# Kernel tuning notes

Measured on AMD Instinct MI355X. Metric: run time of the kernel, lower is better.

Reference implementation:

```python
import jax, jax.numpy as jnp
import numpy as np

H = 4            # num_heads (forced: 128 projection / d_k=32)
DK = 32          # hardcoded d_k
SCALE = 1.0 / np.sqrt(32.0)
EPS = 1e-5       # LayerNorm eps (torch default)


def setup_inputs() -> dict:
    key = jax.random.key(0)
    ks = jax.random.split(key, 8)
    B, L, Dq, Dkv, M = 16, 4096, 512, 512, 512
    def w(k, shape, fan_in):
        return (jax.random.normal(k, shape, jnp.float32) / np.sqrt(fan_in)).astype(jnp.float32)
    return {
        "Q_in":  jax.random.normal(ks[0], (B, L, Dq),  jnp.float32),
        "KV_in": jax.random.normal(ks[1], (B, L, Dkv), jnp.float32),
        "Wq":  w(ks[2], (Dq, 128), Dq),   "bq":  jnp.zeros((128,), jnp.float32),
        "Wk":  w(ks[3], (Dkv, 128), Dkv), "bk":  jnp.zeros((128,), jnp.float32),
        "Wv":  w(ks[4], (Dkv, 128), Dkv), "bv":  jnp.zeros((128,), jnp.float32),
        "Wo":  w(ks[5], (128, M), 128),   "bo":  jnp.zeros((M,), jnp.float32),
        "Wqo": w(ks[6], (128, M), 128),   "bqo": jnp.zeros((M,), jnp.float32),
        "gamma": jnp.ones((M,), jnp.float32),
        "beta":  jnp.zeros((M,), jnp.float32),
    }


def reference(Q_in, KV_in, Wq, bq, Wk, bk, Wv, bv, Wo, bo, Wqo, bqo, gamma, beta):
    B, L, _ = Q_in.shape
    Qm = Q_in @ Wq + bq          # (B, L, 128)
    Km = KV_in @ Wk + bk         # (B, L, 128)
    Vm = KV_in @ Wv + bv         # (B, L, 128)

    def heads(X):
        # view(B, L, H, DK).permute(0, 2, 3, 1) -> (B, H, DK, L)
        return X.reshape(B, L, H, DK).transpose(0, 2, 3, 1)

    Qh, Kh, Vh = heads(Qm), heads(Km), heads(Vm)
    # matmul contracts over the SEQUENCE dim -> feature-feature scores (B,H,DK,DK)
    scores = jnp.einsum('bhdl,bhel->bhde', Qh, Kh) * SCALE
    attn = jax.nn.softmax(scores, axis=-1)          # dropout = identity (eval)
    out_h = jnp.einsum('bhde,bhel->bhdl', attn, Vh)  # (B, H, DK, L)
    out_h = out_h.transpose(0, 3, 1, 2).reshape(B, L, H * DK)  # (B, L, 128)

    out = out_h @ Wo + bo        # (B, L, M)
    Qm_ = Qm @ Wqo + bqo         # (B, L, M)
    x = Qm_ + out
    mu = jnp.mean(x, axis=-1, keepdims=True)
    var = jnp.var(x, axis=-1, keepdims=True)
    y = (x - mu) * jax.lax.rsqrt(var + EPS) * gamma + beta
    return (y, attn)
```

## Files before the change

kernel.cpp:

```cpp
#include <hip/hip_runtime.h>
#include <hip/hip_bf16.h>

typedef __bf16   bf16x8 __attribute__((ext_vector_type(8)));
typedef _Float16 f16x8  __attribute__((ext_vector_type(8)));
typedef float    f32x4  __attribute__((ext_vector_type(4)));

#define SCALE_QK 0.17677669529663687f
#define LDSS 40
#define TL   136

__device__ __forceinline__ float b2f(ushort u) {
    __hip_bfloat16 h; *reinterpret_cast<ushort*>(&h) = u; return __bfloat162float(h);
}
__device__ __forceinline__ ushort f2b(float f) {
    __hip_bfloat16 h = __float2bfloat16(f); return *reinterpret_cast<ushort*>(&h);
}
__device__ __forceinline__ ushort f2h(float f) {
    union { _Float16 h; ushort u; } x; x.h = (_Float16)f; return x.u;
}

__global__ void k_prep(const float* __restrict__ Wq, const float* __restrict__ Wk,
                       const float* __restrict__ Wv, const float* __restrict__ Wqo,
                       const float* __restrict__ Wo,
                       ushort* __restrict__ WqT, ushort* __restrict__ WkT,
                       ushort* __restrict__ WvT, ushort* __restrict__ WqoT,
                       ushort* __restrict__ WoB) {
    int idx = blockIdx.x * 256 + threadIdx.x;
    int mat = idx >> 16, i = idx & 65535;
    if (mat == 0) {
        int n = i >> 9, k = i & 511;
        WqT[i] = f2h(Wq[k * 128 + n]);
    } else if (mat == 1) {
        int n = i >> 9, k = i & 511;
        WkT[i] = f2h(Wk[k * 128 + n]);
    } else if (mat == 2) {
        int n = i >> 9, k = i & 511;
        WvT[i] = f2h(Wv[k * 128 + n]);
    } else if (mat == 3) {
        int n = i >> 7, k = i & 127;
        WqoT[i] = f2b(Wqo[k * 512 + n]);
    } else if (mat == 4) {
        WoB[i] = f2b(Wo[i]);
    }
}

__global__ __launch_bounds__(256) void k_qkv_scores(
        const float* __restrict__ Qin, const float* __restrict__ KVin,
        const ushort* __restrict__ WqT, const ushort* __restrict__ WkT,
        const ushort* __restrict__ WvT,
        const float* __restrict__ bq, const float* __restrict__ bk,
        const float* __restrict__ bv,
        ushort* __restrict__ QmB, ushort* __restrict__ VmB,
        float* __restrict__ partial) {
    __shared__ __align__(16) ushort lds[2 * 128 * TL];
    ushort* P1  = lds;
    ushort* P2  = lds + 128 * TL;
    ushort* As  = P2;
    ushort* Bs0 = P2 + 128 * LDSS;
    ushort* Bs1 = P2 + 2 * 128 * LDSS;

    const int row0 = blockIdx.x * 128;
    const int tid  = threadIdx.x;
    const int wid  = tid >> 6, lane = tid & 63;
    const int wm = wid >> 1, wn = wid & 1;
    const int quad = lane >> 4, l16 = lane & 15;
    const int sr = tid >> 2;
    const int sc = (tid & 3) * 8;

    {
        f32x4 acc[4][4] = {};
        for (int k0 = 0; k0 < 512; k0 += 32) {
            __syncthreads();
#pragma unroll
            for (int p = 0; p < 2; ++p) {
                int r = sr + p * 64;
                float4 a0 = *(const float4*)&Qin[(size_t)(row0 + r) * 512 + k0 + sc];
                float4 a1 = *(const float4*)&Qin[(size_t)(row0 + r) * 512 + k0 + sc + 4];
                union { uint4 v; ushort u[8]; } H;
                H.u[0] = f2h(a0.x); H.u[1] = f2h(a0.y); H.u[2] = f2h(a0.z); H.u[3] = f2h(a0.w);
                H.u[4] = f2h(a1.x); H.u[5] = f2h(a1.y); H.u[6] = f2h(a1.z); H.u[7] = f2h(a1.w);
                *(uint4*)&As[r * LDSS + sc]  = H.v;
                *(uint4*)&Bs0[r * LDSS + sc] = *(const uint4*)&WqT[(size_t)r * 512 + k0 + sc];
            }
            __syncthreads();
            f16x8 aF[4];
#pragma unroll
            for (int i = 0; i < 4; ++i)
                aF[i] = *reinterpret_cast<const f16x8*>(&As[(wm * 64 + i * 16 + l16) * LDSS + quad * 8]);
#pragma unroll
            for (int j = 0; j < 4; ++j) {
                f16x8 bF = *reinterpret_cast<const f16x8*>(&Bs0[(wn * 64 + j * 16 + l16) * LDSS + quad * 8]);
#pragma unroll
                for (int i = 0; i < 4; ++i)
                    acc[i][j] = __builtin_amdgcn_mfma_f32_16x16x32_f16(aF[i], bF, acc[i][j], 0, 0, 0);
            }
        }
#pragma unroll
        for (int j = 0; j < 4; ++j) {
            int col = wn * 64 + j * 16 + l16;
            float bqv = bq[col];
#pragma unroll
            for (int i = 0; i < 4; ++i)
#pragma unroll
                for (int r = 0; r < 4; ++r) {
                    int row = wm * 64 + i * 16 + quad * 4 + r;
                    float v = acc[i][j][r] + bqv;
                    QmB[(size_t)(row0 + row) * 128 + col] = f2b(v);
                    P1[col * TL + row] = f2h(v);
                }
        }
    }

    {
        f32x4 accK[4][4] = {};
        f32x4 accV[4][4] = {};
        for (int k0 = 0; k0 < 512; k0 += 32) {
            __syncthreads();
#pragma unroll
            for (int p = 0; p < 2; ++p) {
                int r = sr + p * 64;
                float4 a0 = *(const float4*)&KVin[(size_t)(row0 + r) * 512 + k0 + sc];
                float4 a1 = *(const float4*)&KVin[(size_t)(row0 + r) * 512 + k0 + sc + 4];
                union { uint4 v; ushort u[8]; } H;
                H.u[0] = f2h(a0.x); H.u[1] = f2h(a0.y); H.u[2] = f2h(a0.z); H.u[3] = f2h(a0.w);
                H.u[4] = f2h(a1.x); H.u[5] = f2h(a1.y); H.u[6] = f2h(a1.z); H.u[7] = f2h(a1.w);
                *(uint4*)&As[r * LDSS + sc]  = H.v;
                *(uint4*)&Bs0[r * LDSS + sc] = *(const uint4*)&WkT[(size_t)r * 512 + k0 + sc];
                *(uint4*)&Bs1[r * LDSS + sc] = *(const uint4*)&WvT[(size_t)r * 512 + k0 + sc];
            }
            __syncthreads();
            f16x8 aF[4];
#pragma unroll
            for (int i = 0; i < 4; ++i)
                aF[i] = *reinterpret_cast<const f16x8*>(&As[(wm * 64 + i * 16 + l16) * LDSS + quad * 8]);
#pragma unroll
            for (int j = 0; j < 4; ++j) {
                f16x8 bK = *reinterpret_cast<const f16x8*>(&Bs0[(wn * 64 + j * 16 + l16) * LDSS + quad * 8]);
                f16x8 bV = *reinterpret_cast<const f16x8*>(&Bs1[(wn * 64 + j * 16 + l16) * LDSS + quad * 8]);
#pragma unroll
                for (int i = 0; i < 4; ++i) {
                    accK[i][j] = __builtin_amdgcn_mfma_f32_16x16x32_f16(aF[i], bK, accK[i][j], 0, 0, 0);
                    accV[i][j] = __builtin_amdgcn_mfma_f32_16x16x32_f16(aF[i], bV, accV[i][j], 0, 0, 0);
                }
            }
        }
        __syncthreads();
#pragma unroll
        for (int j = 0; j < 4; ++j) {
            int col = wn * 64 + j * 16 + l16;
            float bkv = bk[col], bvv = bv[col];
#pragma unroll
            for (int i = 0; i < 4; ++i)
#pragma unroll
                for (int r = 0; r < 4; ++r) {
                    int row = wm * 64 + i * 16 + quad * 4 + r;
                    float vv = accV[i][j][r] + bvv;
                    VmB[(size_t)(row0 + row) * 128 + col] = f2b(vv);
                    P2[col * TL + row] = f2h(accK[i][j][r] + bkv);
                }
        }
    }
    __syncthreads();

    {
        const int h = wid;
        f32x4 s[2][2] = {};
#pragma unroll
        for (int ks = 0; ks < 4; ++ks) {
            f16x8 qa[2], kb[2];
#pragma unroll
            for (int dt = 0; dt < 2; ++dt)
                qa[dt] = *reinterpret_cast<const f16x8*>(
                    &P1[(h * 32 + dt * 16 + l16) * TL + ks * 32 + quad * 8]);
#pragma unroll
            for (int et = 0; et < 2; ++et)
                kb[et] = *reinterpret_cast<const f16x8*>(
                    &P2[(h * 32 + et * 16 + l16) * TL + ks * 32 + quad * 8]);
#pragma unroll
            for (int dt = 0; dt < 2; ++dt)
#pragma unroll
                for (int et = 0; et < 2; ++et)
                    s[dt][et] = __builtin_amdgcn_mfma_f32_16x16x32_f16(qa[dt], kb[et], s[dt][et], 0, 0, 0);
        }
        const int b = blockIdx.x >> 5, sp = blockIdx.x & 31;
        float* P = partial + (size_t)(sp * 64 + b * 4 + h) * 1024;
#pragma unroll
        for (int dt = 0; dt < 2; ++dt)
#pragma unroll
            for (int et = 0; et < 2; ++et)
#pragma unroll
                for (int r = 0; r < 4; ++r) {
                    int d = dt * 16 + quad * 4 + r, e = et * 16 + l16;
                    P[d * 32 + e] = s[dt][et][r];
                }
    }
}

__global__ __launch_bounds__(256) void k_attn(
        const float* __restrict__ partial, const ushort* __restrict__ WoB,
        float* __restrict__ attnOut, ushort* __restrict__ WcT) {
    int bh = blockIdx.x; int b = bh >> 2, h = bh & 3;
    __shared__ float aS[1024];
    __shared__ __align__(16) ushort wS[32 * 512];
    int t = threadIdx.x;
    for (int i = t; i < 1024; i += 256) {
        float s = 0.f;
#pragma unroll
        for (int sp = 0; sp < 32; ++sp)
            s += partial[(size_t)(sp * 64 + bh) * 1024 + i];
        aS[i] = s * SCALE_QK;
    }
    for (int i = t; i < 2048; i += 256) {
        int r = i >> 6, c = (i & 63) * 8;
        *(uint4*)&wS[r * 512 + c] = *(const uint4*)&WoB[(size_t)(h * 32 + r) * 512 + c];
    }
    __syncthreads();
    if (t < 32) {
        float m = -1e30f;
#pragma unroll
        for (int e = 0; e < 32; ++e) m = fmaxf(m, aS[t * 32 + e]);
        float p[32]; float sum = 0.f;
#pragma unroll
        for (int e = 0; e < 32; ++e) { p[e] = __expf(aS[t * 32 + e] - m); sum += p[e]; }
        float inv = 1.f / sum;
#pragma unroll
        for (int e = 0; e < 32; ++e) aS[t * 32 + e] = p[e] * inv;
    }
    __syncthreads();
    for (int i = t; i < 1024; i += 256)
        attnOut[(size_t)bh * 1024 + i] = aS[i];
    int e = t & 31, mg = t >> 5;
    for (int mi = 0; mi < 64; ++mi) {
        int m = mg * 64 + mi;
        float acc = 0.f;
#pragma unroll
        for (int d = 0; d < 32; ++d)
            acc += aS[d * 32 + e] * b2f(wS[d * 512 + m]);
        WcT[((size_t)b * 512 + m) * 128 + h * 32 + e] = f2b(acc);
    }
}

__global__ __launch_bounds__(256) void k_out_ln(
        const ushort* __restrict__ Vm, const ushort* __restrict__ Qm,
        const ushort* __restrict__ WcT, const ushort* __restrict__ WqoT,
        const float* __restrict__ bo, const float* __restrict__ bqo,
        const float* __restrict__ gamma, const float* __restrict__ beta,
        float* __restrict__ Y) {
    __shared__ __align__(16) ushort As[64 * LDSS];
    __shared__ __align__(16) ushort Bs[512 * LDSS];
    __shared__ float sumS[4][64], sumSS[4][64], muA[64], rsA[64];
    const int row0 = blockIdx.x * 64;
    const int b = row0 >> 12;
    const ushort* WcTb = WcT + (size_t)b * 512 * 128;
    const int tid = threadIdx.x;
    const int wid = tid >> 6, lane = tid & 63;
    const int quad = lane >> 4, l16 = lane & 15;
    const int sr = tid >> 2;
    const int sc = (tid & 3) * 8;

    f32x4 acc[4][8] = {};

    for (int k0 = 0; k0 < 256; k0 += 32) {
        const ushort* Asrc; const ushort* Bsrc; int kk;
        if (k0 < 128) { Asrc = Vm; Bsrc = WcTb; kk = k0; }
        else          { Asrc = Qm; Bsrc = WqoT; kk = k0 - 128; }
        __syncthreads();
        *(uint4*)&As[sr * LDSS + sc] =
            *(const uint4*)&Asrc[(size_t)(row0 + sr) * 128 + kk + sc];
#pragma unroll
        for (int p = 0; p < 8; ++p) {
            int r = sr + p * 64;
            *(uint4*)&Bs[r * LDSS + sc] = *(const uint4*)&Bsrc[(size_t)r * 128 + kk + sc];
        }
        __syncthreads();
        bf16x8 aF[4];
#pragma unroll
        for (int i = 0; i < 4; ++i)
            aF[i] = *reinterpret_cast<const bf16x8*>(&As[(i * 16 + l16) * LDSS + quad * 8]);
#pragma unroll
        for (int j = 0; j < 8; ++j) {
            bf16x8 bF = *reinterpret_cast<const bf16x8*>(
                &Bs[(wid * 128 + j * 16 + l16) * LDSS + quad * 8]);
#pragma unroll
            for (int i = 0; i < 4; ++i)
                acc[i][j] = __builtin_amdgcn_mfma_f32_16x16x32_bf16(aF[i], bF, acc[i][j], 0, 0, 0);
        }
    }

    float bv[8];
#pragma unroll
    for (int j = 0; j < 8; ++j) {
        int ncol = wid * 128 + j * 16 + l16;
        bv[j] = bo[ncol] + bqo[ncol];
    }
    float sArr[4][4], ssArr[4][4];
#pragma unroll
    for (int i = 0; i < 4; ++i)
#pragma unroll
        for (int r = 0; r < 4; ++r) {
            float s = 0.f, ss = 0.f;
#pragma unroll
            for (int j = 0; j < 8; ++j) {
                float x = acc[i][j][r] + bv[j];
                s += x; ss += x * x;
            }
            sArr[i][r] = s; ssArr[i][r] = ss;
        }
#pragma unroll
    for (int off = 1; off < 16; off <<= 1)
#pragma unroll
        for (int i = 0; i < 4; ++i)
#pragma unroll
            for (int r = 0; r < 4; ++r) {
                sArr[i][r]  += __shfl_xor(sArr[i][r],  off, 64);
                ssArr[i][r] += __shfl_xor(ssArr[i][r], off, 64);
            }
    if (l16 == 0) {
#pragma unroll
        for (int i = 0; i < 4; ++i)
#pragma unroll
            for (int r = 0; r < 4; ++r) {
                int row = i * 16 + quad * 4 + r;
                sumS[wid][row]  = sArr[i][r];
                sumSS[wid][row] = ssArr[i][r];
            }
    }
    __syncthreads();
    if (tid < 64) {
        float s = sumS[0][tid] + sumS[1][tid] + sumS[2][tid] + sumS[3][tid];
        float ss = sumSS[0][tid] + sumSS[1][tid] + sumSS[2][tid] + sumSS[3][tid];
        float mu = s * (1.f / 512.f);
        float var = ss * (1.f / 512.f) - mu * mu;
        muA[tid] = mu;
        rsA[tid] = rsqrtf(var + 1e-5f);
    }
    __syncthreads();

    float gj[8], bj[8];
#pragma unroll
    for (int j = 0; j < 8; ++j) {
        int ncol = wid * 128 + j * 16 + l16;
        gj[j] = gamma[ncol]; bj[j] = beta[ncol];
    }
#pragma unroll
    for (int i = 0; i < 4; ++i)
#pragma unroll
        for (int r = 0; r < 4; ++r) {
            int row = i * 16 + quad * 4 + r;
            float mu = muA[row], rstd = rsA[row];
            size_t base = (size_t)(row0 + row) * 512 + wid * 128 + l16;
#pragma unroll
            for (int j = 0; j < 8; ++j) {
                float x = acc[i][j][r] + bv[j];
                Y[base + j * 16] = (x - mu) * rstd * gj[j] + bj[j];
            }
        }
}

extern "C" void kernel_launch(void* const* d_in, const int* in_sizes, int n_in,
                              void* d_out, int out_size, void* d_ws, size_t ws_size,
                              hipStream_t stream) {
    const float* Qin   = (const float*)d_in[0];
    const float* KVin  = (const float*)d_in[1];
    const float* Wq    = (const float*)d_in[2];
    const float* bq    = (const float*)d_in[3];
    const float* Wk    = (const float*)d_in[4];
    const float* bk    = (const float*)d_in[5];
    const float* Wv    = (const float*)d_in[6];
    const float* bv    = (const float*)d_in[7];
    const float* Wo    = (const float*)d_in[8];
    const float* bo    = (const float*)d_in[9];
    const float* Wqo   = (const float*)d_in[10];
    const float* bqo   = (const float*)d_in[11];
    const float* gamma = (const float*)d_in[12];
    const float* beta  = (const float*)d_in[13];
    float* out = (float*)d_out;
    float* attnOut = out + 33554432;

    char* ws = (char*)d_ws;
    ushort* WqT  = (ushort*)(ws);
    ushort* WkT  = (ushort*)(ws + 131072);
    ushort* WvT  = (ushort*)(ws + 262144);
    ushort* WqoT = (ushort*)(ws + 393216);
    ushort* WoB  = (ushort*)(ws + 524288);
    ushort* QmB  = (ushort*)(ws + 655360);
    ushort* VmB  = (ushort*)(ws + 17432576);
    float*  part = (float*) (ws + 34209792);
    ushort* WcT  = (ushort*)(ws + 42598400);

    k_prep<<<1280, 256, 0, stream>>>(Wq, Wk, Wv, Wqo, Wo,
                                     WqT, WkT, WvT, WqoT, WoB);
    k_qkv_scores<<<512, 256, 0, stream>>>(Qin, KVin, WqT, WkT, WvT,
                                          bq, bk, bv, QmB, VmB, part);
    k_attn<<<64, 256, 0, stream>>>(part, WoB, attnOut, WcT);
    k_out_ln<<<1024, 256, 0, stream>>>(VmB, QmB, WcT, WqoT, bo, bqo, gamma, beta, out);
}
```

Baseline: 434.5 us.

## Load GEMM fragments directly from global memory and parallelize attn softmax kernel

Removes LDS staging and the per-k-step barriers in the QKV projection and output/LayerNorm GEMMs, so each wave loads its MFMA fragments straight from global memory (with f32-to-f16 conversion in registers). This drops the sync and LDS traffic cost but gives up LDS data sharing, so waves in the same block reload the same A/B rows, leaning on L1/L2. The attn kernel is split across 4 blocks along the output dimension, its softmax is spread over all threads with shuffles, and it caches the attention column in registers and the Wo slice in LDS as float.

```diff
diff --git a/kernel.cpp b/kernel.cpp
--- a/kernel.cpp
+++ b/kernel.cpp
@@ -6,7 +6,6 @@
 typedef float    f32x4  __attribute__((ext_vector_type(4)));
 
 #define SCALE_QK 0.17677669529663687f
-#define LDSS 40
 #define TL   136
 
 __device__ __forceinline__ float b2f(ushort u) {
@@ -17,6 +16,12 @@
 }
 __device__ __forceinline__ ushort f2h(float f) {
     union { _Float16 h; ushort u; } x; x.h = (_Float16)f; return x.u;
+}
+__device__ __forceinline__ f16x8 cvt8f(float4 a, float4 b) {
+    union { f16x8 v; ushort u[8]; } H;
+    H.u[0] = f2h(a.x); H.u[1] = f2h(a.y); H.u[2] = f2h(a.z); H.u[3] = f2h(a.w);
+    H.u[4] = f2h(b.x); H.u[5] = f2h(b.y); H.u[6] = f2h(b.z); H.u[7] = f2h(b.w);
+    return H.v;
 }
 
 __global__ void k_prep(const float* __restrict__ Wq, const float* __restrict__ Wk,
@@ -53,43 +58,29 @@
         ushort* __restrict__ QmB, ushort* __restrict__ VmB,
         float* __restrict__ partial) {
     __shared__ __align__(16) ushort lds[2 * 128 * TL];
-    ushort* P1  = lds;
-    ushort* P2  = lds + 128 * TL;
-    ushort* As  = P2;
-    ushort* Bs0 = P2 + 128 * LDSS;
-    ushort* Bs1 = P2 + 2 * 128 * LDSS;
+    ushort* P1 = lds;
+    ushort* P2 = lds + 128 * TL;
 
     const int row0 = blockIdx.x * 128;
     const int tid  = threadIdx.x;
     const int wid  = tid >> 6, lane = tid & 63;
     const int wm = wid >> 1, wn = wid & 1;
     const int quad = lane >> 4, l16 = lane & 15;
-    const int sr = tid >> 2;
-    const int sc = (tid & 3) * 8;
 
     {
         f32x4 acc[4][4] = {};
+#pragma unroll 4
         for (int k0 = 0; k0 < 512; k0 += 32) {
-            __syncthreads();
-#pragma unroll
-            for (int p = 0; p < 2; ++p) {
-                int r = sr + p * 64;
-                float4 a0 = *(const float4*)&Qin[(size_t)(row0 + r) * 512 + k0 + sc];
-                float4 a1 = *(const float4*)&Qin[(size_t)(row0 + r) * 512 + k0 + sc + 4];
-                union { uint4 v; ushort u[8]; } H;
-                H.u[0] = f2h(a0.x); H.u[1] = f2h(a0.y); H.u[2] = f2h(a0.z); H.u[3] = f2h(a0.w);
-                H.u[4] = f2h(a1.x); H.u[5] = f2h(a1.y); H.u[6] = f2h(a1.z); H.u[7] = f2h(a1.w);
-                *(uint4*)&As[r * LDSS + sc]  = H.v;
-                *(uint4*)&Bs0[r * LDSS + sc] = *(const uint4*)&WqT[(size_t)r * 512 + k0 + sc];
-            }
-            __syncthreads();
             f16x8 aF[4];
 #pragma unroll
-            for (int i = 0; i < 4; ++i)
-                aF[i] = *reinterpret_cast<const f16x8*>(&As[(wm * 64 + i * 16 + l16) * LDSS + quad * 8]);
+            for (int i = 0; i < 4; ++i) {
+                const float* p = Qin + (size_t)(row0 + wm * 64 + i * 16 + l16) * 512 + k0 + quad * 8;
+                aF[i] = cvt8f(*(const float4*)p, *(const float4*)(p + 4));
+            }
 #pragma unroll
             for (int j = 0; j < 4; ++j) {
-                f16x8 bF = *reinterpret_cast<const f16x8*>(&Bs0[(wn * 64 + j * 16 + l16) * LDSS + quad * 8]);
+                f16x8 bF = *reinterpret_cast<const f16x8*>(
+                    &WqT[(size_t)(wn * 64 + j * 16 + l16) * 512 + k0 + quad * 8]);
 #pragma unroll
                 for (int i = 0; i < 4; ++i)
                     acc[i][j] = __builtin_amdgcn_mfma_f32_16x16x32_f16(aF[i], bF, acc[i][j], 0, 0, 0);
@@ -114,29 +105,20 @@
     {
         f32x4 accK[4][4] = {};
         f32x4 accV[4][4] = {};
+#pragma unroll 4
         for (int k0 = 0; k0 < 512; k0 += 32) {
-            __syncthreads();
-#pragma unroll
-            for (int p = 0; p < 2; ++p) {
-                int r = sr + p * 64;
-                float4 a0 = *(const float4*)&KVin[(size_t)(row0 + r) * 512 + k0 + sc];
-                float4 a1 = *(const float4*)&KVin[(size_t)(row0 + r) * 512 + k0 + sc + 4];
-                union { uint4 v; ushort u[8]; } H;
-                H.u[0] = f2h(a0.x); H.u[1] = f2h(a0.y); H.u[2] = f2h(a0.z); H.u[3] = f2h(a0.w);
-                H.u[4] = f2h(a1.x); H.u[5] = f2h(a1.y); H.u[6] = f2h(a1.z); H.u[7] = f2h(a1.w);
-                *(uint4*)&As[r * LDSS + sc]  = H.v;
-                *(uint4*)&Bs0[r * LDSS + sc] = *(const uint4*)&WkT[(size_t)r * 512 + k0 + sc];
-                *(uint4*)&Bs1[r * LDSS + sc] = *(const uint4*)&WvT[(size_t)r * 512 + k0 + sc];
-            }
-            __syncthreads();
             f16x8 aF[4];
 #pragma unroll
-            for (int i = 0; i < 4; ++i)
-                aF[i] = *reinterpret_cast<const f16x8*>(&As[(wm * 64 + i * 16 + l16) * LDSS + quad * 8]);
+            for (int i = 0; i < 4; ++i) {
+                const float* p = KVin + (size_t)(row0 + wm * 64 + i * 16 + l16) * 512 + k0 + quad * 8;
+                aF[i] = cvt8f(*(const float4*)p, *(const float4*)(p + 4));
+            }
 #pragma unroll
             for (int j = 0; j < 4; ++j) {
-                f16x8 bK = *reinterpret_cast<const f16x8*>(&Bs0[(wn * 64 + j * 16 + l16) * LDSS + quad * 8]);
-                f16x8 bV = *reinterpret_cast<const f16x8*>(&Bs1[(wn * 64 + j * 16 + l16) * LDSS + quad * 8]);
+                f16x8 bK = *reinterpret_cast<const f16x8*>(
+                    &WkT[(size_t)(wn * 64 + j * 16 + l16) * 512 + k0 + quad * 8]);
+                f16x8 bV = *reinterpret_cast<const f16x8*>(
+                    &WvT[(size_t)(wn * 64 + j * 16 + l16) * 512 + k0 + quad * 8]);
 #pragma unroll
                 for (int i = 0; i < 4; ++i) {
                     accK[i][j] = __builtin_amdgcn_mfma_f32_16x16x32_f16(aF[i], bK, accK[i][j], 0, 0, 0);
@@ -144,7 +126,6 @@
                 }
             }
         }
-        __syncthreads();
 #pragma unroll
         for (int j = 0; j < 4; ++j) {
             int col = wn * 64 + j * 16 + l16;
@@ -200,8 +181,9 @@
         const float* __restrict__ partial, const ushort* __restrict__ WoB,
         float* __restrict__ attnOut, ushort* __restrict__ WcT) {
     int bh = blockIdx.x; int b = bh >> 2, h = bh & 3;
+    int mq = blockIdx.y;
     __shared__ float aS[1024];
-    __shared__ __align__(16) ushort wS[32 * 512];
+    __shared__ float wSf[32 * 128];
     int t = threadIdx.x;
     for (int i = t; i < 1024; i += 256) {
         float s = 0.f;
@@ -210,32 +192,46 @@
             s += partial[(size_t)(sp * 64 + bh) * 1024 + i];
         aS[i] = s * SCALE_QK;
     }
-    for (int i = t; i < 2048; i += 256) {
-        int r = i >> 6, c = (i & 63) * 8;
-        *(uint4*)&wS[r * 512 + c] = *(const uint4*)&WoB[(size_t)(h * 32 + r) * 512 + c];
-    }
-    __syncthreads();
-    if (t < 32) {
-        float m = -1e30f;
-#pragma unroll
-        for (int e = 0; e < 32; ++e) m = fmaxf(m, aS[t * 32 + e]);
-        float p[32]; float sum = 0.f;
-#pragma unroll
-        for (int e = 0; e < 32; ++e) { p[e] = __expf(aS[t * 32 + e] - m); sum += p[e]; }
-        float inv = 1.f / sum;
-#pragma unroll
-        for (int e = 0; e < 32; ++e) aS[t * 32 + e] = p[e] * inv;
-    }
-    __syncthreads();
-    for (int i = t; i < 1024; i += 256)
-        attnOut[(size_t)bh * 1024 + i] = aS[i];
+    for (int i = t; i < 4096; i += 256) {
+        int r = i >> 7, c = i & 127;
+        wSf[i] = b2f(WoB[(size_t)(h * 32 + r) * 512 + mq * 128 + c]);
+    }
+    __syncthreads();
+    {
+        int row = t >> 3, sub = t & 7;
+        float v[4];
+#pragma unroll
+        for (int z = 0; z < 4; ++z) v[z] = aS[row * 32 + sub * 4 + z];
+        float m = fmaxf(fmaxf(v[0], v[1]), fmaxf(v[2], v[3]));
+#pragma unroll
+        for (int off = 1; off < 8; off <<= 1)
+            m = fmaxf(m, __shfl_xor(m, off, 64));
+        float pz[4], s = 0.f;
+#pragma unroll
+        for (int z = 0; z < 4; ++z) { pz[z] = __expf(v[z] - m); s += pz[z]; }
+#pragma unroll
+        for (int off = 1; off < 8; off <<= 1)
+            s += __shfl_xor(s, off, 64);
+        float inv = 1.f / s;
+#pragma unroll
+        for (int z = 0; z < 4; ++z) aS[row * 32 + sub * 4 + z] = pz[z] * inv;
+    }
+    __syncthreads();
+    if (mq == 0)
+        for (int i = t; i < 1024; i += 256)
+            attnOut[(size_t)bh * 1024 + i] = aS[i];
     int e = t & 31, mg = t >> 5;
-    for (int mi = 0; mi < 64; ++mi) {
-        int m = mg * 64 + mi;
+    float prow[32];
+#pragma unroll
+    for (int d = 0; d < 32; ++d) prow[d] = aS[d * 32 + e];
+#pragma unroll 4
+    for (int mi = 0; mi < 16; ++mi) {
+        int ml = mg * 16 + mi;
         float acc = 0.f;
 #pragma unroll
         for (int d = 0; d < 32; ++d)
-            acc += aS[d * 32 + e] * b2f(wS[d * 512 + m]);
+            acc += prow[d] * wSf[d * 128 + ml];
+        int m = mq * 128 + ml;
         WcT[((size_t)b * 512 + m) * 128 + h * 32 + e] = f2b(acc);
     }
 }
@@ -246,8 +242,6 @@
         const float* __restrict__ bo, const float* __restrict__ bqo,
         const float* __restrict__ gamma, const float* __restrict__ beta,
         float* __restrict__ Y) {
-    __shared__ __align__(16) ushort As[64 * LDSS];
-    __shared__ __align__(16) ushort Bs[512 * LDSS];
     __shared__ float sumS[4][64], sumSS[4][64], muA[64], rsA[64];
     const int row0 = blockIdx.x * 64;
     const int b = row0 >> 12;
@@ -255,35 +249,31 @@
     const int tid = threadIdx.x;
     const int wid = tid >> 6, lane = tid & 63;
     const int quad = lane >> 4, l16 = lane & 15;
-    const int sr = tid >> 2;
-    const int sc = (tid & 3) * 8;
 
     f32x4 acc[4][8] = {};
 
-    for (int k0 = 0; k0 < 256; k0 += 32) {
-        const ushort* Asrc; const ushort* Bsrc; int kk;
-        if (k0 < 128) { Asrc = Vm; Bsrc = WcTb; kk = k0; }
-        else          { Asrc = Qm; Bsrc = WqoT; kk = k0 - 128; }
-        __syncthreads();
-        *(uint4*)&As[sr * LDSS + sc] =
-            *(const uint4*)&Asrc[(size_t)(row0 + sr) * 128 + kk + sc];
-#pragma unroll
-        for (int p = 0; p < 8; ++p) {
-            int r = sr + p * 64;
-            *(uint4*)&Bs[r * LDSS + sc] = *(const uint4*)&Bsrc[(size_t)r * 128 + kk + sc];
-        }
-        __syncthreads();
-        bf16x8 aF[4];
-#pragma unroll
-        for (int i = 0; i < 4; ++i)
-            aF[i] = *reinterpret_cast<const bf16x8*>(&As[(i * 16 + l16) * LDSS + quad * 8]);
-#pragma unroll
-        for (int j = 0; j < 8; ++j) {
-            bf16x8 bF = *reinterpret_cast<const bf16x8*>(
-                &Bs[(wid * 128 + j * 16 + l16) * LDSS + quad * 8]);
+    const ushort* Asrc[2] = { Vm, Qm };
+    const ushort* Bsrc[2] = { WcTb, WqoT };
+#pragma unroll
+    for (int half = 0; half < 2; ++half) {
+        const ushort* A = Asrc[half];
+        const ushort* B = Bsrc[half];
+#pragma unroll 2
+        for (int ks = 0; ks < 4; ++ks) {
+            int kk = ks * 32;
+            bf16x8 aF[4];
 #pragma unroll
             for (int i = 0; i < 4; ++i)
-                acc[i][j] = __builtin_amdgcn_mfma_f32_16x16x32_bf16(aF[i], bF, acc[i][j], 0, 0, 0);
+                aF[i] = *reinterpret_cast<const bf16x8*>(
+                    &A[(size_t)(row0 + i * 16 + l16) * 128 + kk + quad * 8]);
+#pragma unroll
+            for (int j = 0; j < 8; ++j) {
+                bf16x8 bF = *reinterpret_cast<const bf16x8*>(
+                    &B[(size_t)(wid * 128 + j * 16 + l16) * 128 + kk + quad * 8]);
+#pragma unroll
+                for (int i = 0; i < 4; ++i)
+                    acc[i][j] = __builtin_amdgcn_mfma_f32_16x16x32_bf16(aF[i], bF, acc[i][j], 0, 0, 0);
+            }
         }
     }
 
@@ -392,6 +382,6 @@
                                      WqT, WkT, WvT, WqoT, WoB);
     k_qkv_scores<<<512, 256, 0, stream>>>(Qin, KVin, WqT, WkT, WvT,
                                           bq, bk, bv, QmB, VmB, part);
-    k_attn<<<64, 256, 0, stream>>>(part, WoB, attnOut, WcT);
+    k_attn<<<dim3(64, 4), 256, 0, stream>>>(part, WoB, attnOut, WcT);
     k_out_ln<<<1024, 256, 0, stream>>>(VmB, QmB, WcT, WqoT, bo, bqo, gamma, beta, out);
 }
```

After: 562.7 us. +29.5%, slower.
